# Performance work log

Measured on AMD Instinct MI355X. Metric: run time of the kernel, lower is better.

Reference implementation:

```python
import jax, jax.numpy as jnp
import numpy as np

N_NODES = 100000
N_EDGES = 1600000
D_IN = 128
D_OUT = 128


def setup_inputs() -> dict:
    key = jax.random.key(0)
    k1, k2, k3, k4, k5, k6 = jax.random.split(key, 6)
    x = jax.random.normal(k1, (N_NODES, D_IN), dtype=jnp.float32)
    row = jnp.sort(jax.random.randint(k2, (N_EDGES,), 0, N_NODES, dtype=jnp.int32))
    col = jax.random.randint(k3, (N_EDGES,), 0, N_NODES, dtype=jnp.int32)
    val = jax.random.uniform(k4, (N_EDGES,), dtype=jnp.float32)
    # Glorot init for the two linear weights (stored as [in, out] for x @ W)
    std_l = float(np.sqrt(6.0 / (D_IN + D_OUT)))
    W_l = jax.random.uniform(k5, (D_IN, D_OUT), minval=-std_l, maxval=std_l, dtype=jnp.float32)
    b_l = jnp.zeros((D_OUT,), dtype=jnp.float32)
    W_r = jax.random.uniform(k6, (D_IN, D_OUT), minval=-std_l, maxval=std_l, dtype=jnp.float32)
    return {"x": x, "row": row, "col": col, "val": val, "W_l": W_l, "b_l": b_l, "W_r": W_r}


def reference(x, row, col, val, W_l, b_l, W_r):
    n = x.shape[0]
    # out_l = graph @ x  (sparse COO matmul: gather source feats, scale, scatter-add to rows)
    msg = val[:, None] * x[col]                      # [E, D_in]
    out_l = jax.ops.segment_sum(msg, row, num_segments=n)  # [N, D_in]
    # lin_l(out_l) + lin_r(x)
    return out_l @ W_l + b_l + x @ W_r
```

## Files before the change

kernel.cpp:

```cpp
#include <hip/hip_runtime.h>

#define D 128
#define EDGE_CAP 1024
typedef unsigned int uint32;
typedef __bf16 bf16x8 __attribute__((ext_vector_type(8)));
typedef float f32x4 __attribute__((ext_vector_type(4)));

__device__ __forceinline__ unsigned short f2bf(float f) {
    unsigned u = __float_as_uint(f);
    unsigned r = u + 0x7FFFu + ((u >> 16) & 1u);
    return (unsigned short)(r >> 16);
}
__device__ __forceinline__ float bflo(uint32 u) { return __uint_as_float(u << 16); }
__device__ __forceinline__ float bfhi(uint32 u) { return __uint_as_float(u & 0xFFFF0000u); }

__device__ __forceinline__ void fma8(float* acc, uint4 r, float v) {
    acc[0] += v * bflo(r.x); acc[1] += v * bfhi(r.x);
    acc[2] += v * bflo(r.y); acc[3] += v * bfhi(r.y);
    acc[4] += v * bflo(r.z); acc[5] += v * bfhi(r.z);
    acc[6] += v * bflo(r.w); acc[7] += v * bfhi(r.w);
}

__global__ __launch_bounds__(256) void prep_kernel(
    const float* __restrict__ x, unsigned short* __restrict__ xh, int n8,
    const int* __restrict__ row, int* __restrict__ row_ptr,
    int n_nodes, int n_edges,
    const float* __restrict__ Wl, const float* __restrict__ Wr,
    unsigned short* __restrict__ Wlt, unsigned short* __restrict__ Wrt,
    int nbConv, int nbRp) {
    const int b = blockIdx.x;
    if (b < nbConv) {
        const int id = b * 256 + threadIdx.x;
        if (id < n8) {
            const float4* p = (const float4*)x + (size_t)id * 2;
            float4 a = p[0], bb = p[1];
            uint4 o;
            o.x = f2bf(a.x) | ((uint32)f2bf(a.y) << 16);
            o.y = f2bf(a.z) | ((uint32)f2bf(a.w) << 16);
            o.z = f2bf(bb.x) | ((uint32)f2bf(bb.y) << 16);
            o.w = f2bf(bb.z) | ((uint32)f2bf(bb.w) << 16);
            ((uint4*)xh)[id] = o;
        }
    } else if (b < nbConv + nbRp) {
        const int e = (b - nbConv) * 256 + threadIdx.x;
        if (e < n_edges) {
            const int r = row[e];
            const int rp = (e == 0) ? -1 : row[e - 1];
            for (int n = rp + 1; n <= r; ++n) row_ptr[n] = e;
            if (e == n_edges - 1)
                for (int n = r + 1; n <= n_nodes; ++n) row_ptr[n] = n_edges;
        }
    } else {
        const int id = (b - nbConv - nbRp) * 256 + threadIdx.x;
        if (id < 16384) {
            const int n = id & 127, k = id >> 7;
            Wlt[n * 128 + k] = f2bf(Wl[k * 128 + n]);
            Wrt[n * 128 + k] = f2bf(Wr[k * 128 + n]);
        }
    }
}

__global__ __launch_bounds__(256) void spmm_bf16_kernel(
    const unsigned short* __restrict__ xh,
    const int* __restrict__ row_ptr,
    const int* __restrict__ col,
    const float* __restrict__ val,
    unsigned short* __restrict__ outlh, int n_nodes) {
    __shared__ int   sc[EDGE_CAP];
    __shared__ float sv[EDGE_CAP];
    const int tid = threadIdx.x;
    const int n0 = blockIdx.x * 16;
    const int e0 = row_ptr[n0];
    const int e1 = row_ptr[min(n0 + 16, n_nodes)];
    const int ne = min(e1 - e0, EDGE_CAP);
    for (int t = tid; t < ne; t += 256) {
        sc[t] = col[e0 + t];
        sv[t] = val[e0 + t];
    }
    __syncthreads();

    const int wv = tid >> 6, lane = tid & 63;
    const int g = lane >> 4, lq = lane & 15;
    const int n = n0 + wv * 4 + g;
    const int q8 = lq * 8;

    int s = 0, e = 0;
    if (n < n_nodes) { s = row_ptr[n]; e = row_ptr[n + 1]; }

    float acc[8] = {0.f, 0.f, 0.f, 0.f, 0.f, 0.f, 0.f, 0.f};

    auto fetch = [&](int idx, int& c, float& v) {
        if (idx < e) {
            const int li = idx - e0;
            if (li < EDGE_CAP) { c = sc[li]; v = sv[li]; }
            else               { c = col[idx]; v = val[idx]; }
        } else { c = 0; v = 0.f; }
    };

    int i = s;
    int c0, c1, c2, c3; float v0, v1, v2, v3;
    fetch(i + 0, c0, v0); fetch(i + 1, c1, v1);
    fetch(i + 2, c2, v2); fetch(i + 3, c3, v3);
    uint4 r0 = *(const uint4*)&xh[c0 * D + q8];
    uint4 r1 = *(const uint4*)&xh[c1 * D + q8];
    uint4 r2 = *(const uint4*)&xh[c2 * D + q8];
    uint4 r3 = *(const uint4*)&xh[c3 * D + q8];

    while (i < e) {
        const int i2 = i + 4;
        int d0, d1, d2, d3; float w0, w1, w2, w3;
        fetch(i2 + 0, d0, w0); fetch(i2 + 1, d1, w1);
        fetch(i2 + 2, d2, w2); fetch(i2 + 3, d3, w3);
        const uint4 t0 = *(const uint4*)&xh[d0 * D + q8];
        const uint4 t1 = *(const uint4*)&xh[d1 * D + q8];
        const uint4 t2 = *(const uint4*)&xh[d2 * D + q8];
        const uint4 t3 = *(const uint4*)&xh[d3 * D + q8];
        fma8(acc, r0, v0);
        fma8(acc, r1, v1);
        fma8(acc, r2, v2);
        fma8(acc, r3, v3);
        r0 = t0; r1 = t1; r2 = t2; r3 = t3;
        v0 = w0; v1 = w1; v2 = w2; v3 = w3;
        i = i2;
    }

    if (n < n_nodes) {
        uint4 o;
        o.x = f2bf(acc[0]) | ((uint32)f2bf(acc[1]) << 16);
        o.y = f2bf(acc[2]) | ((uint32)f2bf(acc[3]) << 16);
        o.z = f2bf(acc[4]) | ((uint32)f2bf(acc[5]) << 16);
        o.w = f2bf(acc[6]) | ((uint32)f2bf(acc[7]) << 16);
        *(uint4*)&outlh[n * D + q8] = o;
    }
}

__global__ __launch_bounds__(256) void gemm_mfma_kernel(
    const unsigned short* __restrict__ xh,
    const unsigned short* __restrict__ outlh,
    const unsigned short* __restrict__ Wlt,
    const unsigned short* __restrict__ Wrt,
    const float* __restrict__ b_l,
    float* __restrict__ out, int M) {
    const int tid = threadIdx.x;
    const int wid = tid >> 6, lane = tid & 63;
    const int wm = wid >> 1, wn = wid & 1;
    const int m0 = blockIdx.x * 64 + wm * 32;
    const int n0 = wn * 64;
    const int fr = lane & 15;
    const int kofs = (lane >> 4) * 8;

    f32x4 acc[2][4];
#pragma unroll
    for (int mr = 0; mr < 2; ++mr)
#pragma unroll
        for (int nr = 0; nr < 4; ++nr) acc[mr][nr] = (f32x4){0.f, 0.f, 0.f, 0.f};

#pragma unroll
    for (int s = 0; s < 8; ++s) {
        const unsigned short* Abase = (s < 4) ? outlh : xh;
        const unsigned short* Wbase = (s < 4) ? Wlt : Wrt;
        const int k0 = (s & 3) * 32;
        bf16x8 a[2], b[4];
#pragma unroll
        for (int mr = 0; mr < 2; ++mr)
            a[mr] = *(const bf16x8*)&Abase[(m0 + mr * 16 + fr) * D + k0 + kofs];
#pragma unroll
        for (int nr = 0; nr < 4; ++nr)
            b[nr] = *(const bf16x8*)&Wbase[(n0 + nr * 16 + fr) * D + k0 + kofs];
#pragma unroll
        for (int mr = 0; mr < 2; ++mr)
#pragma unroll
            for (int nr = 0; nr < 4; ++nr)
                acc[mr][nr] = __builtin_amdgcn_mfma_f32_16x16x32_bf16(
                    a[mr], b[nr], acc[mr][nr], 0, 0, 0);
    }

    const int r0 = (lane >> 4) * 4;
#pragma unroll
    for (int nr = 0; nr < 4; ++nr) {
        const int ncol = n0 + nr * 16 + fr;
        const float bias = b_l[ncol];
#pragma unroll
        for (int mr = 0; mr < 2; ++mr) {
#pragma unroll
            for (int j = 0; j < 4; ++j) {
                const int m = m0 + mr * 16 + r0 + j;
                if (m < M) out[m * D + ncol] = acc[mr][nr][j] + bias;
            }
        }
    }
}

__global__ void build_rowptr_kernel(const int* __restrict__ row,
                                    int* __restrict__ row_ptr,
                                    int n_nodes, int n_edges) {
    int e = blockIdx.x * blockDim.x + threadIdx.x;
    if (e >= n_edges) return;
    int r = row[e];
    int rp = (e == 0) ? -1 : row[e - 1];
    for (int n = rp + 1; n <= r; ++n) row_ptr[n] = e;
    if (e == n_edges - 1)
        for (int n = r + 1; n <= n_nodes; ++n) row_ptr[n] = n_edges;
}

__global__ __launch_bounds__(128) void spmm_kernel(
    const float* __restrict__ x, const int* __restrict__ row_ptr,
    const int* __restrict__ col, const float* __restrict__ val,
    float* __restrict__ out_l) {
    const int n = blockIdx.x;
    const int d = threadIdx.x;
    const int start = row_ptr[n];
    const int end = row_ptr[n + 1];
    float acc = 0.0f;
    for (int e = start; e < end; ++e)
        acc += val[e] * x[(size_t)col[e] * D + d];
    out_l[(size_t)n * D + d] = acc;
}

__global__ __launch_bounds__(256) void fused_gemm_kernel(
    const float* __restrict__ xin, const float* __restrict__ W_l,
    const float* __restrict__ b_l, const float* __restrict__ W_r,
    float* __restrict__ out, int M) {
    __shared__ float As[64][68];
    __shared__ float Ws[64][132];
    const int tid = threadIdx.x;
    const int tx = tid & 15;
    const int ty = tid >> 4;
    const int ty4 = ty * 4;
    const int m0 = blockIdx.x * 64;
    float acc[4][8];
#pragma unroll
    for (int i = 0; i < 4; ++i)
#pragma unroll
        for (int j = 0; j < 8; ++j) acc[i][j] = 0.0f;
    for (int kt = 0; kt < 4; ++kt) {
        const float* Asrc = (kt < 2) ? out : xin;
        const float* Wsrc = (kt < 2) ? W_l : W_r;
        const int koff = (kt & 1) * 64;
        __syncthreads();
#pragma unroll
        for (int r = 0; r < 4; ++r) {
            const int idx = tid + r * 256;
            const int m = idx >> 4;
            const int kq = idx & 15;
            float4 a = make_float4(0.f, 0.f, 0.f, 0.f);
            if (m0 + m < M)
                a = *(const float4*)&Asrc[(size_t)(m0 + m) * D + koff + kq * 4];
            *(float4*)&As[m][kq * 4] = a;
        }
#pragma unroll
        for (int r = 0; r < 8; ++r) {
            const int idx = tid + r * 256;
            const int k = idx >> 5;
            const int j4 = idx & 31;
            *(float4*)&Ws[k][j4 * 4] =
                *(const float4*)&Wsrc[(size_t)(koff + k) * D + j4 * 4];
        }
        __syncthreads();
#pragma unroll 4
        for (int k = 0; k < 64; ++k) {
            const float a0 = As[ty4 + 0][k], a1 = As[ty4 + 1][k];
            const float a2 = As[ty4 + 2][k], a3 = As[ty4 + 3][k];
            const float4 w0 = *(const float4*)&Ws[k][tx * 4];
            const float4 w1 = *(const float4*)&Ws[k][64 + tx * 4];
            acc[0][0] += a0 * w0.x; acc[0][1] += a0 * w0.y; acc[0][2] += a0 * w0.z; acc[0][3] += a0 * w0.w;
            acc[0][4] += a0 * w1.x; acc[0][5] += a0 * w1.y; acc[0][6] += a0 * w1.z; acc[0][7] += a0 * w1.w;
            acc[1][0] += a1 * w0.x; acc[1][1] += a1 * w0.y; acc[1][2] += a1 * w0.z; acc[1][3] += a1 * w0.w;
            acc[1][4] += a1 * w1.x; acc[1][5] += a1 * w1.y; acc[1][6] += a1 * w1.z; acc[1][7] += a1 * w1.w;
            acc[2][0] += a2 * w0.x; acc[2][1] += a2 * w0.y; acc[2][2] += a2 * w0.z; acc[2][3] += a2 * w0.w;
            acc[2][4] += a2 * w1.x; acc[2][5] += a2 * w1.y; acc[2][6] += a2 * w1.z; acc[2][7] += a2 * w1.w;
            acc[3][0] += a3 * w0.x; acc[3][1] += a3 * w0.y; acc[3][2] += a3 * w0.z; acc[3][3] += a3 * w0.w;
            acc[3][4] += a3 * w1.x; acc[3][5] += a3 * w1.y; acc[3][6] += a3 * w1.z; acc[3][7] += a3 * w1.w;
        }
    }
    const float4 bv0 = *(const float4*)&b_l[tx * 4];
    const float4 bv1 = *(const float4*)&b_l[64 + tx * 4];
#pragma unroll
    for (int i = 0; i < 4; ++i) {
        const int m = m0 + ty4 + i;
        if (m < M) {
            float4 o0, o1;
            o0.x = acc[i][0] + bv0.x; o0.y = acc[i][1] + bv0.y;
            o0.z = acc[i][2] + bv0.z; o0.w = acc[i][3] + bv0.w;
            o1.x = acc[i][4] + bv1.x; o1.y = acc[i][5] + bv1.y;
            o1.z = acc[i][6] + bv1.z; o1.w = acc[i][7] + bv1.w;
            *(float4*)&out[(size_t)m * D + tx * 4] = o0;
            *(float4*)&out[(size_t)m * D + 64 + tx * 4] = o1;
        }
    }
}

static inline size_t align256(size_t x) { return (x + 255) & ~(size_t)255; }

extern "C" void kernel_launch(void* const* d_in, const int* in_sizes, int n_in,
                              void* d_out, int out_size, void* d_ws, size_t ws_size,
                              hipStream_t stream) {
    const float* x   = (const float*)d_in[0];
    const int*   row = (const int*)d_in[1];
    const int*   col = (const int*)d_in[2];
    const float* val = (const float*)d_in[3];
    const float* W_l = (const float*)d_in[4];
    const float* b_l = (const float*)d_in[5];
    const float* W_r = (const float*)d_in[6];
    float* out = (float*)d_out;

    const int n_nodes = in_sizes[0] / D;
    const int n_edges = in_sizes[1];

    const size_t xh_bytes   = (size_t)n_nodes * D * 2;
    const size_t outl_bytes = (size_t)n_nodes * D * 2;
    const size_t wt_bytes   = (size_t)D * D * 2;
    const size_t rp_bytes   = (size_t)(n_nodes + 1) * 4;
    size_t off = 0;
    const size_t xh_off   = off; off += align256(xh_bytes);
    const size_t outl_off = off; off += align256(outl_bytes);
    const size_t wlt_off  = off; off += align256(wt_bytes);
    const size_t wrt_off  = off; off += align256(wt_bytes);
    const size_t rp_off   = off; off += align256(rp_bytes);
    const size_t needed   = off + 65536;

    if (ws_size >= needed) {
        unsigned short* xh    = (unsigned short*)((char*)d_ws + xh_off);
        unsigned short* outlh = (unsigned short*)((char*)d_ws + outl_off);
        unsigned short* Wlt   = (unsigned short*)((char*)d_ws + wlt_off);
        unsigned short* Wrt   = (unsigned short*)((char*)d_ws + wrt_off);
        int* row_ptr          = (int*)((char*)d_ws + rp_off);

        const int n8 = n_nodes * D / 8;
        const int nbConv = (n8 + 255) / 256;
        const int nbRp   = (n_edges + 255) / 256;
        const int nbW    = 64;
        prep_kernel<<<nbConv + nbRp + nbW, 256, 0, stream>>>(
            x, xh, n8, row, row_ptr, n_nodes, n_edges,
            W_l, W_r, Wlt, Wrt, nbConv, nbRp);
        spmm_bf16_kernel<<<(n_nodes + 15) / 16, 256, 0, stream>>>(
            xh, row_ptr, col, val, outlh, n_nodes);
        gemm_mfma_kernel<<<(n_nodes + 63) / 64, 256, 0, stream>>>(
            xh, outlh, Wlt, Wrt, b_l, out, n_nodes);
    } else {
        int* row_ptr = (int*)d_ws;
        build_rowptr_kernel<<<(n_edges + 255) / 256, 256, 0, stream>>>(
            row, row_ptr, n_nodes, n_edges);
        spmm_kernel<<<n_nodes, 128, 0, stream>>>(x, row_ptr, col, val, out);
        fused_gemm_kernel<<<(n_nodes + 63) / 64, 256, 0, stream>>>(
            x, W_l, b_l, W_r, out, n_nodes);
    }
}
```

Baseline: 125.1 us.

## Stage SpMM neighbor row gathers into LDS via async global_load_lds pipeline

Replaces the register-prefetched gather of neighbor feature rows in the SpMM kernel with asynchronous global-to-LDS loads (global_load_lds) into a 4-slot per-wave ring buffer, keeping three stages in flight and waiting on vmcnt before consuming each one. Column indices and values are packed into a single int2 shared array. Blocks whose edge count exceeds the LDS cap fall back to a simple serial loop. The goal is deeper memory-level parallelism with lower register pressure, at the cost of extra LDS traffic, wave-uniform step counts based on the maximum degree among the wave's nodes, and a fragile hand-coded waitcnt encoding.

```diff
diff --git a/kernel.cpp b/kernel.cpp
--- a/kernel.cpp
+++ b/kernel.cpp
@@ -5,6 +5,8 @@
 typedef unsigned int uint32;
 typedef __bf16 bf16x8 __attribute__((ext_vector_type(8)));
 typedef float f32x4 __attribute__((ext_vector_type(4)));
+typedef __attribute__((address_space(1))) const void* gas_ptr;
+typedef __attribute__((address_space(3))) void* las_ptr;
 
 __device__ __forceinline__ unsigned short f2bf(float f) {
     unsigned u = __float_as_uint(f);
@@ -66,62 +68,75 @@
     const int* __restrict__ col,
     const float* __restrict__ val,
     unsigned short* __restrict__ outlh, int n_nodes) {
-    __shared__ int   sc[EDGE_CAP];
-    __shared__ float sv[EDGE_CAP];
+    __shared__ int2 scv[EDGE_CAP];
+    __shared__ char gbuf[4][4][2048];
     const int tid = threadIdx.x;
     const int n0 = blockIdx.x * 16;
     const int e0 = row_ptr[n0];
     const int e1 = row_ptr[min(n0 + 16, n_nodes)];
-    const int ne = min(e1 - e0, EDGE_CAP);
-    for (int t = tid; t < ne; t += 256) {
-        sc[t] = col[e0 + t];
-        sv[t] = val[e0 + t];
+    const int ne = e1 - e0;
+    const bool fits = (ne <= EDGE_CAP);
+    if (fits) {
+        for (int t = tid; t < ne; t += 256)
+            scv[t] = make_int2(col[e0 + t], __float_as_int(val[e0 + t]));
     }
     __syncthreads();
 
     const int wv = tid >> 6, lane = tid & 63;
     const int g = lane >> 4, lq = lane & 15;
     const int n = n0 + wv * 4 + g;
-    const int q8 = lq * 8;
-
     int s = 0, e = 0;
     if (n < n_nodes) { s = row_ptr[n]; e = row_ptr[n + 1]; }
+    const int deg = e - s;
+    const int ls = s - e0;
 
     float acc[8] = {0.f, 0.f, 0.f, 0.f, 0.f, 0.f, 0.f, 0.f};
 
-    auto fetch = [&](int idx, int& c, float& v) {
-        if (idx < e) {
-            const int li = idx - e0;
-            if (li < EDGE_CAP) { c = sc[li]; v = sv[li]; }
-            else               { c = col[idx]; v = val[idx]; }
-        } else { c = 0; v = 0.f; }
-    };
-
-    int i = s;
-    int c0, c1, c2, c3; float v0, v1, v2, v3;
-    fetch(i + 0, c0, v0); fetch(i + 1, c1, v1);
-    fetch(i + 2, c2, v2); fetch(i + 3, c3, v3);
-    uint4 r0 = *(const uint4*)&xh[c0 * D + q8];
-    uint4 r1 = *(const uint4*)&xh[c1 * D + q8];
-    uint4 r2 = *(const uint4*)&xh[c2 * D + q8];
-    uint4 r3 = *(const uint4*)&xh[c3 * D + q8];
-
-    while (i < e) {
-        const int i2 = i + 4;
-        int d0, d1, d2, d3; float w0, w1, w2, w3;
-        fetch(i2 + 0, d0, w0); fetch(i2 + 1, d1, w1);
-        fetch(i2 + 2, d2, w2); fetch(i2 + 3, d3, w3);
-        const uint4 t0 = *(const uint4*)&xh[d0 * D + q8];
-        const uint4 t1 = *(const uint4*)&xh[d1 * D + q8];
-        const uint4 t2 = *(const uint4*)&xh[d2 * D + q8];
-        const uint4 t3 = *(const uint4*)&xh[d3 * D + q8];
-        fma8(acc, r0, v0);
-        fma8(acc, r1, v1);
-        fma8(acc, r2, v2);
-        fma8(acc, r3, v3);
-        r0 = t0; r1 = t1; r2 = t2; r3 = t3;
-        v0 = w0; v1 = w1; v2 = w2; v3 = w3;
-        i = i2;
+    if (fits) {
+        int mdeg = deg;
+        mdeg = max(mdeg, __shfl_xor(mdeg, 16, 64));
+        mdeg = max(mdeg, __shfl_xor(mdeg, 32, 64));
+        const int steps = (mdeg + 1) >> 1;
+
+        const char* xb = (const char*)xh;
+        char* wbuf = &gbuf[wv][0][0];
+        const unsigned co = (unsigned)lq * 16u;
+
+        auto fc = [&](int j) -> int2 {
+            return (j < deg) ? scv[ls + j] : make_int2(0, 0);
+        };
+        auto stage = [&](int T, int k) {
+            const int2 p0 = fc(2 * T), p1 = fc(2 * T + 1);
+            const char* s0 = xb + (size_t)((unsigned)p0.x) * 256u + co;
+            const char* s1 = xb + (size_t)((unsigned)p1.x) * 256u + co;
+            __builtin_amdgcn_global_load_lds((gas_ptr)s0,
+                (las_ptr)(wbuf + k * 2048), 16, 0, 0);
+            __builtin_amdgcn_global_load_lds((gas_ptr)s1,
+                (las_ptr)(wbuf + k * 2048 + 1024), 16, 0, 0);
+        };
+
+        stage(0, 0); stage(1, 1); stage(2, 2);
+
+        for (int T = 0; T < steps; ++T) {
+            const int k = T & 3;
+            __builtin_amdgcn_s_waitcnt(0x0F74);
+            __builtin_amdgcn_sched_barrier(0);
+            const int2 p0 = fc(2 * T), p1 = fc(2 * T + 1);
+            const uint4 r0 = *(const uint4*)(wbuf + k * 2048 + g * 256 + lq * 16);
+            const uint4 r1 = *(const uint4*)(wbuf + k * 2048 + 1024 + g * 256 + lq * 16);
+            fma8(acc, r0, __int_as_float(p0.y));
+            fma8(acc, r1, __int_as_float(p1.y));
+            stage(T + 3, (T + 3) & 3);
+        }
+        __builtin_amdgcn_s_waitcnt(0x0F70);
+        __builtin_amdgcn_sched_barrier(0);
+    } else {
+        for (int j = 0; j < deg; ++j) {
+            const int c = col[s + j];
+            const float v = val[s + j];
+            const uint4 r = *(const uint4*)&xh[(size_t)c * D + lq * 8];
+            fma8(acc, r, v);
+        }
     }
 
     if (n < n_nodes) {
@@ -130,7 +145,7 @@
         o.y = f2bf(acc[2]) | ((uint32)f2bf(acc[3]) << 16);
         o.z = f2bf(acc[4]) | ((uint32)f2bf(acc[5]) << 16);
         o.w = f2bf(acc[6]) | ((uint32)f2bf(acc[7]) << 16);
-        *(uint4*)&outlh[n * D + q8] = o;
+        *(uint4*)&outlh[(size_t)n * D + lq * 8] = o;
     }
 }
 
```

Result: slower. 136.4 us (+9.0%).

## Fuse SpMM aggregation and dual-weight MFMA GEMM into one kernel via LDS

Applied to the files above, without the earlier changes.

Merges the bf16 SpMM kernel and the MFMA GEMM kernel into a single kernel. Each 16-node block writes its aggregated rows as bf16 into shared memory next to its own x rows, then runs a 16x128 by 256x128 MFMA product against both transposed weights and writes the final output with bias. This removes the outl intermediate round trip through global memory and one kernel launch. The cost is that each small block reloads the full weight matrices from global or L2, and each wave now produces only a 16-row tile. Column and value are also packed into one int2 LDS array, with a fallback global loop when the block's edges exceed the LDS capacity.

```diff
diff --git a/kernel.cpp b/kernel.cpp
--- a/kernel.cpp
+++ b/kernel.cpp
@@ -60,133 +60,129 @@
     }
 }
 
-__global__ __launch_bounds__(256) void spmm_bf16_kernel(
+__global__ __launch_bounds__(256) void spmm_gemm_kernel(
     const unsigned short* __restrict__ xh,
     const int* __restrict__ row_ptr,
     const int* __restrict__ col,
     const float* __restrict__ val,
-    unsigned short* __restrict__ outlh, int n_nodes) {
-    __shared__ int   sc[EDGE_CAP];
-    __shared__ float sv[EDGE_CAP];
+    const unsigned short* __restrict__ Wlt,
+    const unsigned short* __restrict__ Wrt,
+    const float* __restrict__ b_l,
+    float* __restrict__ out, int n_nodes) {
+    __shared__ int2 scv[EDGE_CAP];
+    __shared__ unsigned short A_lds[16][264];
     const int tid = threadIdx.x;
     const int n0 = blockIdx.x * 16;
     const int e0 = row_ptr[n0];
     const int e1 = row_ptr[min(n0 + 16, n_nodes)];
-    const int ne = min(e1 - e0, EDGE_CAP);
-    for (int t = tid; t < ne; t += 256) {
-        sc[t] = col[e0 + t];
-        sv[t] = val[e0 + t];
+    const int ne = e1 - e0;
+    const bool fits = (ne <= EDGE_CAP);
+    if (fits) {
+        for (int t = tid; t < ne; t += 256)
+            scv[t] = make_int2(col[e0 + t], __float_as_int(val[e0 + t]));
+    }
+
+    {
+        const int r = tid >> 4, ch = tid & 15;
+        uint4 v = make_uint4(0u, 0u, 0u, 0u);
+        if (n0 + r < n_nodes)
+            v = *(const uint4*)&xh[(size_t)(n0 + r) * D + ch * 8];
+        *(uint4*)&A_lds[r][128 + ch * 8] = v;
     }
     __syncthreads();
 
     const int wv = tid >> 6, lane = tid & 63;
     const int g = lane >> 4, lq = lane & 15;
-    const int n = n0 + wv * 4 + g;
-    const int q8 = lq * 8;
+    const int nloc = wv * 4 + g;
+    const int n = n0 + nloc;
 
     int s = 0, e = 0;
     if (n < n_nodes) { s = row_ptr[n]; e = row_ptr[n + 1]; }
 
     float acc[8] = {0.f, 0.f, 0.f, 0.f, 0.f, 0.f, 0.f, 0.f};
 
-    auto fetch = [&](int idx, int& c, float& v) {
-        if (idx < e) {
-            const int li = idx - e0;
-            if (li < EDGE_CAP) { c = sc[li]; v = sv[li]; }
-            else               { c = col[idx]; v = val[idx]; }
-        } else { c = 0; v = 0.f; }
-    };
-
-    int i = s;
-    int c0, c1, c2, c3; float v0, v1, v2, v3;
-    fetch(i + 0, c0, v0); fetch(i + 1, c1, v1);
-    fetch(i + 2, c2, v2); fetch(i + 3, c3, v3);
-    uint4 r0 = *(const uint4*)&xh[c0 * D + q8];
-    uint4 r1 = *(const uint4*)&xh[c1 * D + q8];
-    uint4 r2 = *(const uint4*)&xh[c2 * D + q8];
-    uint4 r3 = *(const uint4*)&xh[c3 * D + q8];
-
-    while (i < e) {
-        const int i2 = i + 4;
-        int d0, d1, d2, d3; float w0, w1, w2, w3;
-        fetch(i2 + 0, d0, w0); fetch(i2 + 1, d1, w1);
-        fetch(i2 + 2, d2, w2); fetch(i2 + 3, d3, w3);
-        const uint4 t0 = *(const uint4*)&xh[d0 * D + q8];
-        const uint4 t1 = *(const uint4*)&xh[d1 * D + q8];
-        const uint4 t2 = *(const uint4*)&xh[d2 * D + q8];
-        const uint4 t3 = *(const uint4*)&xh[d3 * D + q8];
-        fma8(acc, r0, v0);
-        fma8(acc, r1, v1);
-        fma8(acc, r2, v2);
-        fma8(acc, r3, v3);
-        r0 = t0; r1 = t1; r2 = t2; r3 = t3;
-        v0 = w0; v1 = w1; v2 = w2; v3 = w3;
-        i = i2;
-    }
-
-    if (n < n_nodes) {
+    if (fits) {
+        auto fetch = [&](int idx, int& c, float& v) {
+            if (idx < e) {
+                const int li = idx - e0;
+                if (li < EDGE_CAP) { c = scv[li].x; v = __int_as_float(scv[li].y); }
+                else               { c = col[idx]; v = val[idx]; }
+            } else { c = 0; v = 0.f; }
+        };
+
+        int i = s;
+        int c0, c1, c2, c3; float v0, v1, v2, v3;
+        fetch(i + 0, c0, v0); fetch(i + 1, c1, v1);
+        fetch(i + 2, c2, v2); fetch(i + 3, c3, v3);
+        uint4 r0 = *(const uint4*)&xh[c0 * D + lq * 8];
+        uint4 r1 = *(const uint4*)&xh[c1 * D + lq * 8];
+        uint4 r2 = *(const uint4*)&xh[c2 * D + lq * 8];
+        uint4 r3 = *(const uint4*)&xh[c3 * D + lq * 8];
+
+        while (i < e) {
+            const int i2 = i + 4;
+            int d0, d1, d2, d3; float w0, w1, w2, w3;
+            fetch(i2 + 0, d0, w0); fetch(i2 + 1, d1, w1);
+            fetch(i2 + 2, d2, w2); fetch(i2 + 3, d3, w3);
+            const uint4 t0 = *(const uint4*)&xh[d0 * D + lq * 8];
+            const uint4 t1 = *(const uint4*)&xh[d1 * D + lq * 8];
+            const uint4 t2 = *(const uint4*)&xh[d2 * D + lq * 8];
+            const uint4 t3 = *(const uint4*)&xh[d3 * D + lq * 8];
+            fma8(acc, r0, v0);
+            fma8(acc, r1, v1);
+            fma8(acc, r2, v2);
+            fma8(acc, r3, v3);
+            r0 = t0; r1 = t1; r2 = t2; r3 = t3;
+            v0 = w0; v1 = w1; v2 = w2; v3 = w3;
+            i = i2;
+        }
+    } else {
+        for (int j = s; j < e; ++j) {
+            const int c = col[j];
+            const float v = val[j];
+            const uint4 r = *(const uint4*)&xh[(size_t)c * D + lq * 8];
+            fma8(acc, r, v);
+        }
+    }
+
+    {
         uint4 o;
         o.x = f2bf(acc[0]) | ((uint32)f2bf(acc[1]) << 16);
         o.y = f2bf(acc[2]) | ((uint32)f2bf(acc[3]) << 16);
         o.z = f2bf(acc[4]) | ((uint32)f2bf(acc[5]) << 16);
         o.w = f2bf(acc[6]) | ((uint32)f2bf(acc[7]) << 16);
-        *(uint4*)&outlh[n * D + q8] = o;
-    }
-}
-
-__global__ __launch_bounds__(256) void gemm_mfma_kernel(
-    const unsigned short* __restrict__ xh,
-    const unsigned short* __restrict__ outlh,
-    const unsigned short* __restrict__ Wlt,
-    const unsigned short* __restrict__ Wrt,
-    const float* __restrict__ b_l,
-    float* __restrict__ out, int M) {
-    const int tid = threadIdx.x;
-    const int wid = tid >> 6, lane = tid & 63;
-    const int wm = wid >> 1, wn = wid & 1;
-    const int m0 = blockIdx.x * 64 + wm * 32;
-    const int n0 = wn * 64;
+        *(uint4*)&A_lds[nloc][lq * 8] = o;
+    }
+    __syncthreads();
+
     const int fr = lane & 15;
     const int kofs = (lane >> 4) * 8;
-
-    f32x4 acc[2][4];
-#pragma unroll
-    for (int mr = 0; mr < 2; ++mr)
-#pragma unroll
-        for (int nr = 0; nr < 4; ++nr) acc[mr][nr] = (f32x4){0.f, 0.f, 0.f, 0.f};
-
-#pragma unroll
-    for (int s = 0; s < 8; ++s) {
-        const unsigned short* Abase = (s < 4) ? outlh : xh;
-        const unsigned short* Wbase = (s < 4) ? Wlt : Wrt;
-        const int k0 = (s & 3) * 32;
-        bf16x8 a[2], b[4];
-#pragma unroll
-        for (int mr = 0; mr < 2; ++mr)
-            a[mr] = *(const bf16x8*)&Abase[(m0 + mr * 16 + fr) * D + k0 + kofs];
-#pragma unroll
-        for (int nr = 0; nr < 4; ++nr)
-            b[nr] = *(const bf16x8*)&Wbase[(n0 + nr * 16 + fr) * D + k0 + kofs];
-#pragma unroll
-        for (int mr = 0; mr < 2; ++mr)
-#pragma unroll
-            for (int nr = 0; nr < 4; ++nr)
-                acc[mr][nr] = __builtin_amdgcn_mfma_f32_16x16x32_bf16(
-                    a[mr], b[nr], acc[mr][nr], 0, 0, 0);
-    }
-
-    const int r0 = (lane >> 4) * 4;
-#pragma unroll
-    for (int nr = 0; nr < 4; ++nr) {
-        const int ncol = n0 + nr * 16 + fr;
+    f32x4 acc2[2];
+    acc2[0] = (f32x4){0.f, 0.f, 0.f, 0.f};
+    acc2[1] = (f32x4){0.f, 0.f, 0.f, 0.f};
+#pragma unroll
+    for (int st = 0; st < 8; ++st) {
+        const int k0 = st * 32;
+        const unsigned short* Wsel = (k0 < 128) ? Wlt : Wrt;
+        const int kk = k0 & 127;
+        const bf16x8 a = *(const bf16x8*)&A_lds[fr][k0 + kofs];
+#pragma unroll
+        for (int nr = 0; nr < 2; ++nr) {
+            const int ncol = wv * 32 + nr * 16 + fr;
+            const bf16x8 b = *(const bf16x8*)&Wsel[ncol * 128 + kk + kofs];
+            acc2[nr] = __builtin_amdgcn_mfma_f32_16x16x32_bf16(
+                a, b, acc2[nr], 0, 0, 0);
+        }
+    }
+    const int r0c = (lane >> 4) * 4;
+#pragma unroll
+    for (int nr = 0; nr < 2; ++nr) {
+        const int ncol = wv * 32 + nr * 16 + fr;
         const float bias = b_l[ncol];
 #pragma unroll
-        for (int mr = 0; mr < 2; ++mr) {
-#pragma unroll
-            for (int j = 0; j < 4; ++j) {
-                const int m = m0 + mr * 16 + r0 + j;
-                if (m < M) out[m * D + ncol] = acc[mr][nr][j] + bias;
-            }
+        for (int j = 0; j < 4; ++j) {
+            const int m = n0 + r0c + j;
+            if (m < n_nodes) out[(size_t)m * D + ncol] = acc2[nr][j] + bias;
         }
     }
 }
@@ -307,24 +303,21 @@
     const int n_nodes = in_sizes[0] / D;
     const int n_edges = in_sizes[1];
 
-    const size_t xh_bytes   = (size_t)n_nodes * D * 2;
-    const size_t outl_bytes = (size_t)n_nodes * D * 2;
-    const size_t wt_bytes   = (size_t)D * D * 2;
-    const size_t rp_bytes   = (size_t)(n_nodes + 1) * 4;
+    const size_t xh_bytes = (size_t)n_nodes * D * 2;
+    const size_t wt_bytes = (size_t)D * D * 2;
+    const size_t rp_bytes = (size_t)(n_nodes + 1) * 4;
     size_t off = 0;
-    const size_t xh_off   = off; off += align256(xh_bytes);
-    const size_t outl_off = off; off += align256(outl_bytes);
-    const size_t wlt_off  = off; off += align256(wt_bytes);
-    const size_t wrt_off  = off; off += align256(wt_bytes);
-    const size_t rp_off   = off; off += align256(rp_bytes);
-    const size_t needed   = off + 65536;
+    const size_t xh_off  = off; off += align256(xh_bytes);
+    const size_t wlt_off = off; off += align256(wt_bytes);
+    const size_t wrt_off = off; off += align256(wt_bytes);
+    const size_t rp_off  = off; off += align256(rp_bytes);
+    const size_t needed  = off + 65536;
 
     if (ws_size >= needed) {
-        unsigned short* xh    = (unsigned short*)((char*)d_ws + xh_off);
-        unsigned short* outlh = (unsigned short*)((char*)d_ws + outl_off);
-        unsigned short* Wlt   = (unsigned short*)((char*)d_ws + wlt_off);
-        unsigned short* Wrt   = (unsigned short*)((char*)d_ws + wrt_off);
-        int* row_ptr          = (int*)((char*)d_ws + rp_off);
+        unsigned short* xh  = (unsigned short*)((char*)d_ws + xh_off);
+        unsigned short* Wlt = (unsigned short*)((char*)d_ws + wlt_off);
+        unsigned short* Wrt = (unsigned short*)((char*)d_ws + wrt_off);
+        int* row_ptr        = (int*)((char*)d_ws + rp_off);
 
         const int n8 = n_nodes * D / 8;
         const int nbConv = (n8 + 255) / 256;
@@ -333,10 +326,8 @@
         prep_kernel<<<nbConv + nbRp + nbW, 256, 0, stream>>>(
             x, xh, n8, row, row_ptr, n_nodes, n_edges,
             W_l, W_r, Wlt, Wrt, nbConv, nbRp);
-        spmm_bf16_kernel<<<(n_nodes + 15) / 16, 256, 0, stream>>>(
-            xh, row_ptr, col, val, outlh, n_nodes);
-        gemm_mfma_kernel<<<(n_nodes + 63) / 64, 256, 0, stream>>>(
-            xh, outlh, Wlt, Wrt, b_l, out, n_nodes);
+        spmm_gemm_kernel<<<(n_nodes + 15) / 16, 256, 0, stream>>>(
+            xh, row_ptr, col, val, Wlt, Wrt, b_l, out, n_nodes);
     } else {
         int* row_ptr = (int*)d_ws;
         build_rowptr_kernel<<<(n_edges + 255) / 256, 256, 0, stream>>>(
```

New measurement: 108.9 us (median of 2 runs). 1.15x faster.
